# Performance work log

Measured on AMD Instinct MI355X. Metric: run time of the kernel, lower is better.

## Reference

```python
import jax, jax.numpy as jnp
import numpy as np

EPS = 1e-5  # BatchNorm2d default eps


def _deform_conv(x, offset, W_def, b_def, K):
    # torchvision.ops.DeformConv2d, stride=1, dilation=1, padding=K//2, groups=1
    B, C, H, W = x.shape
    KK = K * K
    pad = K // 2
    # offset channels ordered (y, x) per kernel tap: [B, KK, 2, H, W]
    off = offset.reshape(B, KK, 2, H, W)
    ky = (jnp.arange(KK) // K).astype(x.dtype)
    kx = (jnp.arange(KK) % K).astype(x.dtype)
    base_y = jnp.arange(H, dtype=x.dtype)[None, :, None] - pad + ky[:, None, None]  # [KK,H,1]
    base_x = jnp.arange(W, dtype=x.dtype)[None, None, :] - pad + kx[:, None, None]  # [KK,1,W]
    py = off[:, :, 0] + base_y[None]  # [B,KK,H,W] sampling rows
    px = off[:, :, 1] + base_x[None]  # [B,KK,H,W] sampling cols
    y0 = jnp.floor(py)
    x0 = jnp.floor(px)
    wy = py - y0
    wx = px - x0
    xf = x.reshape(B, C, H * W)

    def corner(iy, ix, w):
        valid = ((iy >= 0) & (iy < H) & (ix >= 0) & (ix < W)).astype(x.dtype)
        idx = jnp.clip(iy, 0, H - 1).astype(jnp.int32) * W + jnp.clip(ix, 0, W - 1).astype(jnp.int32)
        g = jnp.take_along_axis(xf, idx.reshape(B, 1, KK * H * W), axis=2)
        return g.reshape(B, C, KK, H, W) * (w * valid)[:, None]

    sampled = (corner(y0, x0, (1 - wy) * (1 - wx))
               + corner(y0, x0 + 1, (1 - wy) * wx)
               + corner(y0 + 1, x0, wy * (1 - wx))
               + corner(y0 + 1, x0 + 1, wy * wx))  # [B,C,KK,H,W]
    out = jnp.einsum('bckhw,ock->bohw', sampled, W_def.reshape(W_def.shape[0], C, KK))
    return out + b_def[None, :, None, None]


def reference(x, W_off, b_off, W_def, b_def, W_cat, b_cat, gamma, beta):
    K = W_def.shape[-1]
    # 3x3 offset-generating conv, padding=1
    offset = jax.lax.conv_general_dilated(
        x, W_off, (1, 1), ((1, 1), (1, 1)),
        dimension_numbers=('NCHW', 'OIHW', 'NCHW')) + b_off[None, :, None, None]
    y1 = _deform_conv(x, offset, W_def, b_def, K)
    # 1x1 conv
    y = jnp.einsum('bchw,oc->bohw', y1, W_cat) + b_cat[None, :, None, None]
    # BatchNorm2d in training mode (batch statistics, biased var)
    mean = y.mean(axis=(0, 2, 3))
    var = y.var(axis=(0, 2, 3))
    yn = (y - mean[None, :, None, None]) * jax.lax.rsqrt(var + EPS)[None, :, None, None]
    out = jax.nn.relu(gamma[None, :, None, None] * yn + beta[None, :, None, None])
    return out + x


def setup_inputs() -> dict:
    key = jax.random.key(0)
    ks = jax.random.split(key, 5)
    B, C, H, W, K = 4, 64, 192, 192, 3
    return {
        'x': jax.random.normal(ks[0], (B, C, H, W), dtype=jnp.float32),
        'W_off': jax.random.normal(ks[1], (2 * K * K, C, 3, 3), dtype=jnp.float32) * 0.02,
        'b_off': jnp.zeros((2 * K * K,), dtype=jnp.float32),
        'W_def': jax.random.normal(ks[2], (C, C, K, K), dtype=jnp.float32) * (1.0 / np.sqrt(C * K * K)),
        'b_def': jnp.zeros((C,), dtype=jnp.float32),
        'W_cat': jax.random.normal(ks[3], (C, C), dtype=jnp.float32) * (1.0 / np.sqrt(C)),
        'b_cat': jnp.zeros((C,), dtype=jnp.float32),
        'gamma': jnp.ones((C,), dtype=jnp.float32),
        'beta': jnp.zeros((C,), dtype=jnp.float32),
    }
```

## Files before the change

### kernel.cpp

```cpp
#include <hip/hip_runtime.h>
#include <math.h>

constexpr int Hh  = 192;
constexpr int Ww  = 192;
constexpr int HWp = Hh * Ww;
constexpr int Cc  = 64;
constexpr int Bb  = 4;
constexpr int KK  = 9;
constexpr int OFFC = 18;
constexpr int PXB = 32;
constexpr int NBPX = HWp / PXB;
constexpr int KSD = (Cc * KK) / 32;
constexpr int KSC = Cc / 32;
constexpr int NIT = KK * PXB;
constexpr int SLOTS = 64;

constexpr int NXP = Bb * (HWp / 64);
constexpr int NWP = (4 * KSD * 64 * 8 + 4 * KSC * 64 * 8 + 2 * KSD * 64 * 8) / 256;
constexpr int NZP = (2 * Cc * SLOTS / 4) / 256;

using bf16x8 = __attribute__((ext_vector_type(8))) short;
using f32x4  = __attribute__((ext_vector_type(4))) float;

static __device__ __forceinline__ unsigned short f2bf(float f) {
    unsigned int u = __float_as_uint(f);
    u += 0x7fff + ((u >> 16) & 1);
    return (unsigned short)(u >> 16);
}
static __device__ __forceinline__ float bf2f(unsigned short u) {
    return __uint_as_float((unsigned)u << 16);
}

__global__ __launch_bounds__(256)
void k_prep(const float* __restrict__ x, const float* __restrict__ Wdef,
            const float* __restrict__ Wcat, const float* __restrict__ Woff,
            unsigned short* __restrict__ xcl, unsigned short* __restrict__ Fd,
            unsigned short* __restrict__ Fc, unsigned short* __restrict__ Fo,
            float* __restrict__ psum) {
    __shared__ unsigned short tile[64][66];
    const int bid = blockIdx.x;
    const int t = threadIdx.x;
    if (bid < NXP) {
        int b   = bid / (HWp / 64);
        int px0 = (bid % (HWp / 64)) * 64;
        #pragma unroll
        for (int r = 0; r < 4; ++r) {
            int c = r * 16 + (t >> 4), px4 = (t & 15) * 4;
            float4 v = *(const float4*)(x + ((size_t)b * Cc + c) * HWp + px0 + px4);
            tile[c][px4 + 0] = f2bf(v.x);
            tile[c][px4 + 1] = f2bf(v.y);
            tile[c][px4 + 2] = f2bf(v.z);
            tile[c][px4 + 3] = f2bf(v.w);
        }
        __syncthreads();
        #pragma unroll
        for (int r = 0; r < 4; ++r) {
            int pxl = r * 16 + (t >> 4), c4 = (t & 15) * 4;
            ushort4 u;
            u.x = tile[c4 + 0][pxl];
            u.y = tile[c4 + 1][pxl];
            u.z = tile[c4 + 2][pxl];
            u.w = tile[c4 + 3][pxl];
            *(ushort4*)(xcl + ((size_t)b * HWp + px0 + pxl) * Cc + c4) = u;
        }
    } else if (bid < NXP + NWP) {
        int i = (bid - NXP) * 256 + t;
        if (i < 4 * KSD * 64 * 8) {
            int r = i & 7, lane = (i >> 3) & 63, ks = (i >> 9) % KSD, ot = (i >> 9) / KSD;
            int o  = ot * 16 + (lane & 15);
            int kp = ks * 32 + ((lane >> 4) << 3) + r;
            int kk = kp >> 6, c = kp & 63;
            Fd[i] = f2bf(Wdef[o * (Cc * KK) + c * KK + kk]);
        }
        int j = i - 4 * KSD * 64 * 8;
        if (j >= 0 && j < 4 * KSC * 64 * 8) {
            int r = j & 7, lane = (j >> 3) & 63, ks = (j >> 9) & 1, ot = j >> 10;
            int o = ot * 16 + (lane & 15);
            int c = ks * 32 + ((lane >> 4) << 3) + r;
            Fc[j] = f2bf(Wcat[o * Cc + c]);
        }
        int m = j - 4 * KSC * 64 * 8;
        if (m >= 0 && m < 2 * KSD * 64 * 8) {
            int r = m & 7, lane = (m >> 3) & 63, ks = (m >> 9) % KSD, ot = (m >> 9) / KSD;
            int o  = ot * 16 + (lane & 15);
            int kp = ks * 32 + ((lane >> 4) << 3) + r;
            int kk = kp >> 6, c = kp & 63;
            Fo[m] = (o < OFFC) ? f2bf(Woff[o * (Cc * KK) + c * KK + kk]) : 0;
        }
    } else {
        int j = (bid - NXP - NWP) * 256 + t;
        float4 z = {0.f, 0.f, 0.f, 0.f};
        ((float4*)psum)[j] = z;
    }
}

__global__ __launch_bounds__(512)
void k_fused(const unsigned short* __restrict__ xcl,
             const unsigned short* __restrict__ Fo, const float* __restrict__ boff,
             const unsigned short* __restrict__ Fd, const float* __restrict__ bdef,
             const unsigned short* __restrict__ Fc, const float* __restrict__ bcat,
             unsigned short* __restrict__ y, float* __restrict__ psum) {
    __shared__ __align__(16) unsigned char s_buf[PXB * Cc * KK * 2];
    __shared__ __align__(16) unsigned char s_y1[PXB * Cc * 2];
    __shared__ float s_off[PXB][OFFC];
    __shared__ __align__(16) int s_pp[NIT * 8];

    const int t = threadIdx.x;
    const int lane = t & 63, wv = t >> 6;
    const int klane = (lane >> 4) & 3;
    const int c4 = (lane & 15) * 4;
    int wg = blockIdx.x;
    const int slot = wg & (SLOTS - 1);
    wg = (wg & 7) * (Bb * NBPX / 8) + (wg >> 3);
    const int b   = wg / NBPX;
    const int px0 = (wg % NBPX) * PXB;
    const int h   = px0 / Ww;
    const int w0  = px0 % Ww;
    const unsigned short* xb = xcl + (size_t)b * HWp * Cc;

    #pragma unroll
    for (int it = 0; it < NIT / 32; ++it) {
        int item = it * 32 + wv * 4 + klane;
        int kk = item >> 5, pxl = item & 31;
        int ky = (kk * 11) >> 5, kx = kk - ky * 3;
        int row = h + ky - 1;
        int col = w0 + pxl + kx - 1;
        ushort4 u = {0, 0, 0, 0};
        if (row >= 0 && row < Hh && col >= 0 && col < Ww)
            u = *(const ushort4*)(xb + (size_t)(row * Ww + col) * Cc + c4);
        unsigned addr = (unsigned)pxl * (Cc * KK * 2)
                      + ((((unsigned)(kk * 64 + c4)) * 2) ^ ((unsigned)(pxl & 7) << 4));
        *(ushort4*)(s_buf + addr) = u;
    }
    __syncthreads();

    if (wv < 4) {
        const int oto = wv >> 1, pxt = wv & 1;
        const unsigned swz = (unsigned)(lane & 7) << 4;
        const unsigned rA = ((unsigned)(lane & 15) + (unsigned)pxt * 16) * (Cc * KK * 2);
        f32x4 a = {0.f, 0.f, 0.f, 0.f};
        const bf16x8* Bo = (const bf16x8*)Fo + (size_t)oto * KSD * 64;
        #pragma unroll 3
        for (int ks = 0; ks < KSD; ++ks) {
            unsigned cb = ((unsigned)(ks * 64 + klane * 16)) ^ swz;
            bf16x8 af = *(const bf16x8*)(s_buf + rA + cb);
            a = __builtin_amdgcn_mfma_f32_16x16x32_bf16(af, Bo[ks * 64 + lane], a, 0, 0, 0);
        }
        int oc = oto * 16 + (lane & 15);
        if (oc < OFFC) {
            float bv = boff[oc];
            #pragma unroll
            for (int r = 0; r < 4; ++r)
                s_off[pxt * 16 + klane * 4 + r][oc] = a[r] + bv;
        }
    }
    __syncthreads();

    if (t < NIT) {
        int i = t;
        int kk = i >> 5, pxl = i & 31;
        int ky = (kk * 11) >> 5, kx = kk - ky * 3;
        float py  = s_off[pxl][kk * 2]     + (float)(h - 1 + ky);
        float pxf = s_off[pxl][kk * 2 + 1] + (float)(w0 + pxl - 1 + kx);
        float fy0 = floorf(py), fx0 = floorf(pxf);
        float wy = py - fy0, wx = pxf - fx0;
        int iy0 = (int)fy0, ix0 = (int)fx0, iy1 = iy0 + 1, ix1 = ix0 + 1;
        float v00 = (iy0 >= 0 && iy0 < Hh && ix0 >= 0 && ix0 < Ww) ? 1.f : 0.f;
        float v01 = (iy0 >= 0 && iy0 < Hh && ix1 >= 0 && ix1 < Ww) ? 1.f : 0.f;
        float v10 = (iy1 >= 0 && iy1 < Hh && ix0 >= 0 && ix0 < Ww) ? 1.f : 0.f;
        float v11 = (iy1 >= 0 && iy1 < Hh && ix1 >= 0 && ix1 < Ww) ? 1.f : 0.f;
        int cy0 = min(max(iy0, 0), Hh - 1), cy1 = min(max(iy1, 0), Hh - 1);
        int cx0 = min(max(ix0, 0), Ww - 1), cx1 = min(max(ix1, 0), Ww - 1);
        int* pp = &s_pp[i * 8];
        pp[0] = (cy0 * Ww + cx0) * (Cc * 2);
        pp[1] = (cy0 * Ww + cx1) * (Cc * 2);
        pp[2] = (cy1 * Ww + cx0) * (Cc * 2);
        pp[3] = (cy1 * Ww + cx1) * (Cc * 2);
        pp[4] = __float_as_int((1.f - wy) * (1.f - wx) * v00);
        pp[5] = __float_as_int((1.f - wy) * wx * v01);
        pp[6] = __float_as_int(wy * (1.f - wx) * v10);
        pp[7] = __float_as_int(wy * wx * v11);
    }
    __syncthreads();

    const unsigned char* xbB = (const unsigned char*)xb + (size_t)c4 * 2;
    #pragma unroll 3
    for (int it = 0; it < NIT / 32; ++it) {
        int item = it * 32 + wv * 4 + klane;
        int kk = item >> 5, pxl = item & 31;
        const int* pp = &s_pp[item * 8];
        int4   idx = *(const int4*)pp;
        float4 wt  = *(const float4*)(pp + 4);
        ushort4 u00 = *(const ushort4*)(xbB + idx.x);
        ushort4 u01 = *(const ushort4*)(xbB + idx.y);
        ushort4 u10 = *(const ushort4*)(xbB + idx.z);
        ushort4 u11 = *(const ushort4*)(xbB + idx.w);
        float v0 = wt.x * bf2f(u00.x) + wt.y * bf2f(u01.x) + wt.z * bf2f(u10.x) + wt.w * bf2f(u11.x);
        float v1 = wt.x * bf2f(u00.y) + wt.y * bf2f(u01.y) + wt.z * bf2f(u10.y) + wt.w * bf2f(u11.y);
        float v2 = wt.x * bf2f(u00.z) + wt.y * bf2f(u01.z) + wt.z * bf2f(u10.z) + wt.w * bf2f(u11.z);
        float v3 = wt.x * bf2f(u00.w) + wt.y * bf2f(u01.w) + wt.z * bf2f(u10.w) + wt.w * bf2f(u11.w);
        ushort4 o4;
        o4.x = f2bf(v0); o4.y = f2bf(v1); o4.z = f2bf(v2); o4.w = f2bf(v3);
        unsigned addr = (unsigned)pxl * (Cc * KK * 2)
                      + ((((unsigned)(kk * 64 + c4)) * 2) ^ ((unsigned)(pxl & 7) << 4));
        *(ushort4*)(s_buf + addr) = o4;
    }
    __syncthreads();

    const int ot = wv >> 1, pxt = wv & 1;
    const unsigned swzA = (unsigned)(lane & 7) << 4;
    const unsigned rA = ((unsigned)(lane & 15) + (unsigned)pxt * 16) * (Cc * KK * 2);
    f32x4 acc = {0.f, 0.f, 0.f, 0.f};
    const bf16x8* Bd = (const bf16x8*)Fd + (size_t)ot * KSD * 64;
    #pragma unroll 3
    for (int ks = 0; ks < KSD; ++ks) {
        unsigned cb = ((unsigned)(ks * 64 + klane * 16)) ^ swzA;
        bf16x8 a0 = *(const bf16x8*)(s_buf + rA + cb);
        bf16x8 bd = Bd[ks * 64 + lane];
        acc = __builtin_amdgcn_mfma_f32_16x16x32_bf16(a0, bd, acc, 0, 0, 0);
    }
    const int o = ot * 16 + (lane & 15);
    {
        float bv = bdef[o];
        unsigned colb = (unsigned)o * 2;
        #pragma unroll
        for (int r = 0; r < 4; ++r) {
            int row = pxt * 16 + klane * 4 + r;
            unsigned sw = (unsigned)((klane * 4 + r) & 7) << 4;
            *(unsigned short*)(s_y1 + row * (Cc * 2) + (colb ^ sw)) = f2bf(acc[r] + bv);
        }
    }
    __syncthreads();

    f32x4 cacc = {0.f, 0.f, 0.f, 0.f};
    const bf16x8* Bc = (const bf16x8*)Fc + (size_t)ot * KSC * 64;
    const unsigned rY = ((unsigned)(lane & 15) + (unsigned)pxt * 16) * (Cc * 2);
    #pragma unroll
    for (int ks = 0; ks < KSC; ++ks) {
        unsigned cb = ((unsigned)(ks * 64 + klane * 16)) ^ swzA;
        bf16x8 a0 = *(const bf16x8*)(s_y1 + rY + cb);
        bf16x8 bc = Bc[ks * 64 + lane];
        cacc = __builtin_amdgcn_mfma_f32_16x16x32_bf16(a0, bc, cacc, 0, 0, 0);
    }

    float vals[4];
    {
        float bcv = bcat[o];
        #pragma unroll
        for (int r = 0; r < 4; ++r) vals[r] = cacc[r] + bcv;
        float s1 = 0.f, s2 = 0.f;
        #pragma unroll
        for (int j = 0; j < 4; ++j) { s1 += vals[j]; s2 += vals[j] * vals[j]; }
        s1 += __shfl_xor(s1, 16); s1 += __shfl_xor(s1, 32);
        s2 += __shfl_xor(s2, 16); s2 += __shfl_xor(s2, 32);
        if (klane == 0) {
            atomicAdd(&psum[o * SLOTS + slot], s1);
            atomicAdd(&psum[Cc * SLOTS + o * SLOTS + slot], s2);
        }
    }

    __syncthreads();
    {
        unsigned orow = (unsigned)o * (PXB * 4);
        unsigned sw   = (unsigned)(o & 7) << 4;
        #pragma unroll
        for (int r = 0; r < 4; ++r) {
            int p = pxt * 16 + klane * 4 + r;
            *(float*)(s_buf + orow + (((unsigned)p * 4) ^ sw)) = vals[r];
        }
    }
    __syncthreads();
    unsigned short* yb = y + (size_t)b * Cc * HWp + px0;
    {
        int oo = t >> 3, pxq = t & 7;
        float4 v = *(const float4*)(s_buf + (unsigned)oo * (PXB * 4)
                                    + (((unsigned)pxq * 16) ^ ((unsigned)(oo & 7) << 4)));
        ushort4 u;
        u.x = f2bf(v.x); u.y = f2bf(v.y); u.z = f2bf(v.z); u.w = f2bf(v.w);
        *(ushort4*)(yb + (size_t)oo * HWp + pxq * 4) = u;
    }
}

__global__ __launch_bounds__(64)
void k_stats_final(const float* __restrict__ psum, float* __restrict__ stats) {
    int c = threadIdx.x;
    double t1 = 0.0, t2 = 0.0;
    for (int s = 0; s < SLOTS; ++s) {
        t1 += (double)psum[c * SLOTS + s];
        t2 += (double)psum[Cc * SLOTS + c * SLOTS + s];
    }
    double n = (double)(Bb * HWp);
    double mean = t1 / n;
    double var  = t2 / n - mean * mean;
    stats[c]      = (float)mean;
    stats[Cc + c] = (float)(1.0 / sqrt(var + 1e-5));
}

__global__ __launch_bounds__(256)
void k_apply(const unsigned short* __restrict__ y, const float4* __restrict__ x,
             const float* __restrict__ stats, const float* __restrict__ gamma,
             const float* __restrict__ beta, float4* __restrict__ out) {
    int idx = blockIdx.x * 256 + threadIdx.x;
    int c = (idx / (HWp / 4)) % Cc;
    float mean = stats[c], inv = stats[Cc + c];
    float g = gamma[c], bt = beta[c];
    ushort4 yv = *(const ushort4*)(y + (size_t)idx * 4);
    float4 xv = x[idx], o;
    o.x = fmaxf(g * ((bf2f(yv.x) - mean) * inv) + bt, 0.f) + xv.x;
    o.y = fmaxf(g * ((bf2f(yv.y) - mean) * inv) + bt, 0.f) + xv.y;
    o.z = fmaxf(g * ((bf2f(yv.z) - mean) * inv) + bt, 0.f) + xv.z;
    o.w = fmaxf(g * ((bf2f(yv.w) - mean) * inv) + bt, 0.f) + xv.w;
    out[idx] = o;
}

extern "C" void kernel_launch(void* const* d_in, const int* in_sizes, int n_in,
                              void* d_out, int out_size, void* d_ws, size_t ws_size,
                              hipStream_t stream) {
    const float* x     = (const float*)d_in[0];
    const float* Woff  = (const float*)d_in[1];
    const float* boff  = (const float*)d_in[2];
    const float* Wdef  = (const float*)d_in[3];
    const float* bdef  = (const float*)d_in[4];
    const float* Wcat  = (const float*)d_in[5];
    const float* bcat  = (const float*)d_in[6];
    const float* gamma = (const float*)d_in[7];
    const float* beta  = (const float*)d_in[8];
    float* out = (float*)d_out;

    float* ws    = (float*)d_ws;
    float* stats = ws;
    float* psum  = stats + 128;
    unsigned short* y16 = (unsigned short*)(psum + 2 * Cc * SLOTS);
    unsigned short* Fd  = y16 + (size_t)Bb * Cc * HWp;
    unsigned short* Fc  = Fd + 4 * KSD * 64 * 8;
    unsigned short* Fo  = Fc + 4 * KSC * 64 * 8;
    unsigned short* xcl = Fo + 2 * KSD * 64 * 8;

    k_prep<<<dim3(NXP + NWP + NZP), dim3(256), 0, stream>>>(x, Wdef, Wcat, Woff,
                                                            xcl, Fd, Fc, Fo, psum);
    k_fused<<<dim3(Bb * NBPX), dim3(512), 0, stream>>>(xcl, Fo, boff, Fd, bdef, Fc, bcat, y16, psum);
    k_stats_final<<<dim3(1), dim3(64), 0, stream>>>(psum, stats);
    k_apply<<<dim3(Bb * Cc * HWp / 4 / 256), dim3(256), 0, stream>>>(
        y16, (const float4*)x, stats, gamma, beta, (float4*)out);
}
```

Baseline: 221.9 us.

## Shrink fused block to 256 threads, load halo tile, fold stats into apply

The offset conv now stages a 3x34 halo tile of x in shared memory instead of nine im2col copies, cutting global loads for that stage. The fused kernel drops from 512 to 256 threads, so each wave computes two pixel tiles for the deform and 1x1 GEMMs and reuses the B fragments. The separate stats-final kernel is removed and each apply block reduces the 64 partial sums itself. The prep transpose uses packed 32-bit swizzled shared tiles, and bilinear sampling uses 2-wide float vectors. The cost is more redundant stats reduction in apply and fewer threads to hide gather latency.

```diff
diff --git a/kernel.cpp b/kernel.cpp
--- a/kernel.cpp
+++ b/kernel.cpp
@@ -14,6 +14,8 @@
 constexpr int KSC = Cc / 32;
 constexpr int NIT = KK * PXB;
 constexpr int SLOTS = 64;
+constexpr int XT_COLS = PXB + 2;
+constexpr int XT_ITEMS = 3 * XT_COLS;
 
 constexpr int NXP = Bb * (HWp / 64);
 constexpr int NWP = (4 * KSD * 64 * 8 + 4 * KSC * 64 * 8 + 2 * KSD * 64 * 8) / 256;
@@ -21,6 +23,7 @@
 
 using bf16x8 = __attribute__((ext_vector_type(8))) short;
 using f32x4  = __attribute__((ext_vector_type(4))) float;
+using f32x2  = __attribute__((ext_vector_type(2))) float;
 
 static __device__ __forceinline__ unsigned short f2bf(float f) {
     unsigned int u = __float_as_uint(f);
@@ -37,7 +40,7 @@
             unsigned short* __restrict__ xcl, unsigned short* __restrict__ Fd,
             unsigned short* __restrict__ Fc, unsigned short* __restrict__ Fo,
             float* __restrict__ psum) {
-    __shared__ unsigned short tile[64][66];
+    __shared__ unsigned int wtile[64][32];
     const int bid = blockIdx.x;
     const int t = threadIdx.x;
     if (bid < NXP) {
@@ -45,23 +48,29 @@
         int px0 = (bid % (HWp / 64)) * 64;
         #pragma unroll
         for (int r = 0; r < 4; ++r) {
-            int c = r * 16 + (t >> 4), px4 = (t & 15) * 4;
-            float4 v = *(const float4*)(x + ((size_t)b * Cc + c) * HWp + px0 + px4);
-            tile[c][px4 + 0] = f2bf(v.x);
-            tile[c][px4 + 1] = f2bf(v.y);
-            tile[c][px4 + 2] = f2bf(v.z);
-            tile[c][px4 + 3] = f2bf(v.w);
+            int cc = r * 16 + (t >> 4), px4 = (t & 15) * 4;
+            float4 v = *(const float4*)(x + ((size_t)b * Cc + cc) * HWp + px0 + px4);
+            unsigned lo  = (unsigned)f2bf(v.x) | ((unsigned)f2bf(v.y) << 16);
+            unsigned hi2 = (unsigned)f2bf(v.z) | ((unsigned)f2bf(v.w) << 16);
+            unsigned e = (unsigned)(cc & 31);
+            wtile[cc][((unsigned)(px4 >> 1)    ) ^ e] = lo;
+            wtile[cc][((unsigned)(px4 >> 1) + 1) ^ e] = hi2;
         }
         __syncthreads();
         #pragma unroll
         for (int r = 0; r < 4; ++r) {
-            int pxl = r * 16 + (t >> 4), c4 = (t & 15) * 4;
+            int pxl = r * 16 + (t >> 4), c4l = (t & 15) * 4;
+            int hsel = (pxl & 1) * 16;
+            unsigned w0 = wtile[c4l + 0][(unsigned)(pxl >> 1) ^ (unsigned)((c4l + 0) & 31)];
+            unsigned w1 = wtile[c4l + 1][(unsigned)(pxl >> 1) ^ (unsigned)((c4l + 1) & 31)];
+            unsigned w2 = wtile[c4l + 2][(unsigned)(pxl >> 1) ^ (unsigned)((c4l + 2) & 31)];
+            unsigned w3 = wtile[c4l + 3][(unsigned)(pxl >> 1) ^ (unsigned)((c4l + 3) & 31)];
             ushort4 u;
-            u.x = tile[c4 + 0][pxl];
-            u.y = tile[c4 + 1][pxl];
-            u.z = tile[c4 + 2][pxl];
-            u.w = tile[c4 + 3][pxl];
-            *(ushort4*)(xcl + ((size_t)b * HWp + px0 + pxl) * Cc + c4) = u;
+            u.x = (unsigned short)(w0 >> hsel);
+            u.y = (unsigned short)(w1 >> hsel);
+            u.z = (unsigned short)(w2 >> hsel);
+            u.w = (unsigned short)(w3 >> hsel);
+            *(ushort4*)(xcl + ((size_t)b * HWp + px0 + pxl) * Cc + c4l) = u;
         }
     } else if (bid < NXP + NWP) {
         int i = (bid - NXP) * 256 + t;
@@ -94,7 +103,7 @@
     }
 }
 
-__global__ __launch_bounds__(512)
+__global__ __launch_bounds__(256, 3)
 void k_fused(const unsigned short* __restrict__ xcl,
              const unsigned short* __restrict__ Fo, const float* __restrict__ boff,
              const unsigned short* __restrict__ Fd, const float* __restrict__ bdef,
@@ -119,31 +128,34 @@
     const unsigned short* xb = xcl + (size_t)b * HWp * Cc;
 
     #pragma unroll
-    for (int it = 0; it < NIT / 32; ++it) {
-        int item = it * 32 + wv * 4 + klane;
-        int kk = item >> 5, pxl = item & 31;
-        int ky = (kk * 11) >> 5, kx = kk - ky * 3;
-        int row = h + ky - 1;
-        int col = w0 + pxl + kx - 1;
-        ushort4 u = {0, 0, 0, 0};
-        if (row >= 0 && row < Hh && col >= 0 && col < Ww)
-            u = *(const ushort4*)(xb + (size_t)(row * Ww + col) * Cc + c4);
-        unsigned addr = (unsigned)pxl * (Cc * KK * 2)
-                      + ((((unsigned)(kk * 64 + c4)) * 2) ^ ((unsigned)(pxl & 7) << 4));
-        *(ushort4*)(s_buf + addr) = u;
-    }
-    __syncthreads();
-
-    if (wv < 4) {
-        const int oto = wv >> 1, pxt = wv & 1;
-        const unsigned swz = (unsigned)(lane & 7) << 4;
-        const unsigned rA = ((unsigned)(lane & 15) + (unsigned)pxt * 16) * (Cc * KK * 2);
+    for (int it = 0; it < 7; ++it) {
+        int item = it * 16 + wv * 4 + klane;
+        if (item < XT_ITEMS) {
+            int ry = item / XT_COLS, cx = item - ry * XT_COLS;
+            int row = h + ry - 1, col = w0 + cx - 1;
+            ushort4 u = {0, 0, 0, 0};
+            if (row >= 0 && row < Hh && col >= 0 && col < Ww)
+                u = *(const ushort4*)(xb + (size_t)(row * Ww + col) * Cc + c4);
+            unsigned addr = (unsigned)item * 128
+                          + (((unsigned)c4 * 2) ^ (((unsigned)item & 7) << 4));
+            *(ushort4*)(s_buf + addr) = u;
+        }
+    }
+    __syncthreads();
+
+    {
+        const int oto = wv >> 1, pxt0 = wv & 1;
+        const int pxv = (lane & 15) + pxt0 * 16;
         f32x4 a = {0.f, 0.f, 0.f, 0.f};
         const bf16x8* Bo = (const bf16x8*)Fo + (size_t)oto * KSD * 64;
-        #pragma unroll 3
+        #pragma unroll
         for (int ks = 0; ks < KSD; ++ks) {
-            unsigned cb = ((unsigned)(ks * 64 + klane * 16)) ^ swz;
-            bf16x8 af = *(const bf16x8*)(s_buf + rA + cb);
+            const int kk = ks >> 1;
+            const int ky = kk / 3, kx = kk % 3;
+            int row_l = ky * XT_COLS + pxv + kx;
+            unsigned c0b = (unsigned)(((ks & 1) * 32 + klane * 8) * 2);
+            unsigned addr = (unsigned)row_l * 128 + (c0b ^ (((unsigned)row_l & 7) << 4));
+            bf16x8 af = *(const bf16x8*)(s_buf + addr);
             a = __builtin_amdgcn_mfma_f32_16x16x32_bf16(af, Bo[ks * 64 + lane], a, 0, 0, 0);
         }
         int oc = oto * 16 + (lane & 15);
@@ -151,13 +163,12 @@
             float bv = boff[oc];
             #pragma unroll
             for (int r = 0; r < 4; ++r)
-                s_off[pxt * 16 + klane * 4 + r][oc] = a[r] + bv;
-        }
-    }
-    __syncthreads();
-
-    if (t < NIT) {
-        int i = t;
+                s_off[pxt0 * 16 + klane * 4 + r][oc] = a[r] + bv;
+        }
+    }
+    __syncthreads();
+
+    for (int i = t; i < NIT; i += 256) {
         int kk = i >> 5, pxl = i & 31;
         int ky = (kk * 11) >> 5, kx = kk - ky * 3;
         float py  = s_off[pxl][kk * 2]     + (float)(h - 1 + ky);
@@ -184,9 +195,9 @@
     __syncthreads();
 
     const unsigned char* xbB = (const unsigned char*)xb + (size_t)c4 * 2;
-    #pragma unroll 3
-    for (int it = 0; it < NIT / 32; ++it) {
-        int item = it * 32 + wv * 4 + klane;
+    #pragma unroll 6
+    for (int it = 0; it < NIT / 16; ++it) {
+        int item = it * 16 + wv * 4 + klane;
         int kk = item >> 5, pxl = item & 31;
         const int* pp = &s_pp[item * 8];
         int4   idx = *(const int4*)pp;
@@ -195,29 +206,34 @@
         ushort4 u01 = *(const ushort4*)(xbB + idx.y);
         ushort4 u10 = *(const ushort4*)(xbB + idx.z);
         ushort4 u11 = *(const ushort4*)(xbB + idx.w);
-        float v0 = wt.x * bf2f(u00.x) + wt.y * bf2f(u01.x) + wt.z * bf2f(u10.x) + wt.w * bf2f(u11.x);
-        float v1 = wt.x * bf2f(u00.y) + wt.y * bf2f(u01.y) + wt.z * bf2f(u10.y) + wt.w * bf2f(u11.y);
-        float v2 = wt.x * bf2f(u00.z) + wt.y * bf2f(u01.z) + wt.z * bf2f(u10.z) + wt.w * bf2f(u11.z);
-        float v3 = wt.x * bf2f(u00.w) + wt.y * bf2f(u01.w) + wt.z * bf2f(u10.w) + wt.w * bf2f(u11.w);
+        f32x2 lo00 = {bf2f(u00.x), bf2f(u00.y)}, hi00 = {bf2f(u00.z), bf2f(u00.w)};
+        f32x2 lo01 = {bf2f(u01.x), bf2f(u01.y)}, hi01 = {bf2f(u01.z), bf2f(u01.w)};
+        f32x2 lo10 = {bf2f(u10.x), bf2f(u10.y)}, hi10 = {bf2f(u10.z), bf2f(u10.w)};
+        f32x2 lo11 = {bf2f(u11.x), bf2f(u11.y)}, hi11 = {bf2f(u11.z), bf2f(u11.w)};
+        f32x2 vlo = wt.x * lo00 + wt.y * lo01 + wt.z * lo10 + wt.w * lo11;
+        f32x2 vhi = wt.x * hi00 + wt.y * hi01 + wt.z * hi10 + wt.w * hi11;
         ushort4 o4;
-        o4.x = f2bf(v0); o4.y = f2bf(v1); o4.z = f2bf(v2); o4.w = f2bf(v3);
+        o4.x = f2bf(vlo[0]); o4.y = f2bf(vlo[1]); o4.z = f2bf(vhi[0]); o4.w = f2bf(vhi[1]);
         unsigned addr = (unsigned)pxl * (Cc * KK * 2)
                       + ((((unsigned)(kk * 64 + c4)) * 2) ^ ((unsigned)(pxl & 7) << 4));
         *(ushort4*)(s_buf + addr) = o4;
     }
     __syncthreads();
 
-    const int ot = wv >> 1, pxt = wv & 1;
+    const int ot = wv;
     const unsigned swzA = (unsigned)(lane & 7) << 4;
-    const unsigned rA = ((unsigned)(lane & 15) + (unsigned)pxt * 16) * (Cc * KK * 2);
-    f32x4 acc = {0.f, 0.f, 0.f, 0.f};
+    const unsigned rA0  = (unsigned)(lane & 15) * (Cc * KK * 2);
+    const unsigned rA1  = rA0 + 16u * (Cc * KK * 2);
+    f32x4 acc0 = {0.f, 0.f, 0.f, 0.f}, acc1 = {0.f, 0.f, 0.f, 0.f};
     const bf16x8* Bd = (const bf16x8*)Fd + (size_t)ot * KSD * 64;
     #pragma unroll 3
     for (int ks = 0; ks < KSD; ++ks) {
         unsigned cb = ((unsigned)(ks * 64 + klane * 16)) ^ swzA;
-        bf16x8 a0 = *(const bf16x8*)(s_buf + rA + cb);
+        bf16x8 a0 = *(const bf16x8*)(s_buf + rA0 + cb);
+        bf16x8 a1 = *(const bf16x8*)(s_buf + rA1 + cb);
         bf16x8 bd = Bd[ks * 64 + lane];
-        acc = __builtin_amdgcn_mfma_f32_16x16x32_bf16(a0, bd, acc, 0, 0, 0);
+        acc0 = __builtin_amdgcn_mfma_f32_16x16x32_bf16(a0, bd, acc0, 0, 0, 0);
+        acc1 = __builtin_amdgcn_mfma_f32_16x16x32_bf16(a1, bd, acc1, 0, 0, 0);
     }
     const int o = ot * 16 + (lane & 15);
     {
@@ -225,32 +241,36 @@
         unsigned colb = (unsigned)o * 2;
         #pragma unroll
         for (int r = 0; r < 4; ++r) {
-            int row = pxt * 16 + klane * 4 + r;
-            unsigned sw = (unsigned)((klane * 4 + r) & 7) << 4;
-            *(unsigned short*)(s_y1 + row * (Cc * 2) + (colb ^ sw)) = f2bf(acc[r] + bv);
-        }
-    }
-    __syncthreads();
-
-    f32x4 cacc = {0.f, 0.f, 0.f, 0.f};
+            int row0 = klane * 4 + r, row1 = row0 + 16;
+            unsigned sw = (unsigned)(row0 & 7) << 4;
+            *(unsigned short*)(s_y1 + row0 * (Cc * 2) + (colb ^ sw)) = f2bf(acc0[r] + bv);
+            *(unsigned short*)(s_y1 + row1 * (Cc * 2) + (colb ^ sw)) = f2bf(acc1[r] + bv);
+        }
+    }
+    __syncthreads();
+
+    f32x4 c0 = {0.f, 0.f, 0.f, 0.f}, c1 = {0.f, 0.f, 0.f, 0.f};
     const bf16x8* Bc = (const bf16x8*)Fc + (size_t)ot * KSC * 64;
-    const unsigned rY = ((unsigned)(lane & 15) + (unsigned)pxt * 16) * (Cc * 2);
+    const unsigned rY0 = (unsigned)(lane & 15) * (Cc * 2);
+    const unsigned rY1 = rY0 + 16u * (Cc * 2);
     #pragma unroll
     for (int ks = 0; ks < KSC; ++ks) {
         unsigned cb = ((unsigned)(ks * 64 + klane * 16)) ^ swzA;
-        bf16x8 a0 = *(const bf16x8*)(s_y1 + rY + cb);
+        bf16x8 a0 = *(const bf16x8*)(s_y1 + rY0 + cb);
+        bf16x8 a1 = *(const bf16x8*)(s_y1 + rY1 + cb);
         bf16x8 bc = Bc[ks * 64 + lane];
-        cacc = __builtin_amdgcn_mfma_f32_16x16x32_bf16(a0, bc, cacc, 0, 0, 0);
-    }
-
-    float vals[4];
+        c0 = __builtin_amdgcn_mfma_f32_16x16x32_bf16(a0, bc, c0, 0, 0, 0);
+        c1 = __builtin_amdgcn_mfma_f32_16x16x32_bf16(a1, bc, c1, 0, 0, 0);
+    }
+
+    float vals[8];
     {
         float bcv = bcat[o];
         #pragma unroll
-        for (int r = 0; r < 4; ++r) vals[r] = cacc[r] + bcv;
+        for (int r = 0; r < 4; ++r) { vals[r] = c0[r] + bcv; vals[4 + r] = c1[r] + bcv; }
         float s1 = 0.f, s2 = 0.f;
         #pragma unroll
-        for (int j = 0; j < 4; ++j) { s1 += vals[j]; s2 += vals[j] * vals[j]; }
+        for (int j = 0; j < 8; ++j) { s1 += vals[j]; s2 += vals[j] * vals[j]; }
         s1 += __shfl_xor(s1, 16); s1 += __shfl_xor(s1, 32);
         s2 += __shfl_xor(s2, 16); s2 += __shfl_xor(s2, 32);
         if (klane == 0) {
@@ -265,14 +285,16 @@
         unsigned sw   = (unsigned)(o & 7) << 4;
         #pragma unroll
         for (int r = 0; r < 4; ++r) {
-            int p = pxt * 16 + klane * 4 + r;
-            *(float*)(s_buf + orow + (((unsigned)p * 4) ^ sw)) = vals[r];
+            int p0 = klane * 4 + r, p1 = p0 + 16;
+            *(float*)(s_buf + orow + (((unsigned)p0 * 4) ^ sw)) = vals[r];
+            *(float*)(s_buf + orow + (((unsigned)p1 * 4) ^ sw)) = vals[4 + r];
         }
     }
     __syncthreads();
     unsigned short* yb = y + (size_t)b * Cc * HWp + px0;
-    {
-        int oo = t >> 3, pxq = t & 7;
+    #pragma unroll
+    for (int it = 0; it < 2; ++it) {
+        int oo = it * 32 + (t >> 3), pxq = t & 7;
         float4 v = *(const float4*)(s_buf + (unsigned)oo * (PXB * 4)
                                     + (((unsigned)pxq * 16) ^ ((unsigned)(oo & 7) << 4)));
         ushort4 u;
@@ -281,28 +303,32 @@
     }
 }
 
-__global__ __launch_bounds__(64)
-void k_stats_final(const float* __restrict__ psum, float* __restrict__ stats) {
-    int c = threadIdx.x;
-    double t1 = 0.0, t2 = 0.0;
-    for (int s = 0; s < SLOTS; ++s) {
-        t1 += (double)psum[c * SLOTS + s];
-        t2 += (double)psum[Cc * SLOTS + c * SLOTS + s];
-    }
-    double n = (double)(Bb * HWp);
-    double mean = t1 / n;
-    double var  = t2 / n - mean * mean;
-    stats[c]      = (float)mean;
-    stats[Cc + c] = (float)(1.0 / sqrt(var + 1e-5));
-}
-
 __global__ __launch_bounds__(256)
 void k_apply(const unsigned short* __restrict__ y, const float4* __restrict__ x,
-             const float* __restrict__ stats, const float* __restrict__ gamma,
+             const float* __restrict__ psum, const float* __restrict__ gamma,
              const float* __restrict__ beta, float4* __restrict__ out) {
-    int idx = blockIdx.x * 256 + threadIdx.x;
-    int c = (idx / (HWp / 4)) % Cc;
-    float mean = stats[c], inv = stats[Cc + c];
+    __shared__ float smv[2];
+    const int t = threadIdx.x;
+    const int idx = blockIdx.x * 256 + t;
+    const int c = (blockIdx.x * 1024 / HWp) % Cc;
+    if (t < 64) {
+        float s1 = psum[c * SLOTS + t];
+        float s2 = psum[Cc * SLOTS + c * SLOTS + t];
+        #pragma unroll
+        for (int d = 1; d < 64; d <<= 1) {
+            s1 += __shfl_xor(s1, d);
+            s2 += __shfl_xor(s2, d);
+        }
+        if (t == 0) {
+            float n = (float)(Bb * HWp);
+            float mean = s1 / n;
+            float var  = s2 / n - mean * mean;
+            smv[0] = mean;
+            smv[1] = 1.0f / sqrtf(var + 1e-5f);
+        }
+    }
+    __syncthreads();
+    float mean = smv[0], inv = smv[1];
     float g = gamma[c], bt = beta[c];
     ushort4 yv = *(const ushort4*)(y + (size_t)idx * 4);
     float4 xv = x[idx], o;
@@ -328,8 +354,7 @@
     float* out = (float*)d_out;
 
     float* ws    = (float*)d_ws;
-    float* stats = ws;
-    float* psum  = stats + 128;
+    float* psum  = ws;
     unsigned short* y16 = (unsigned short*)(psum + 2 * Cc * SLOTS);
     unsigned short* Fd  = y16 + (size_t)Bb * Cc * HWp;
     unsigned short* Fc  = Fd + 4 * KSD * 64 * 8;
@@ -338,8 +363,7 @@
 
     k_prep<<<dim3(NXP + NWP + NZP), dim3(256), 0, stream>>>(x, Wdef, Wcat, Woff,
                                                             xcl, Fd, Fc, Fo, psum);
-    k_fused<<<dim3(Bb * NBPX), dim3(512), 0, stream>>>(xcl, Fo, boff, Fd, bdef, Fc, bcat, y16, psum);
-    k_stats_final<<<dim3(1), dim3(64), 0, stream>>>(psum, stats);
+    k_fused<<<dim3(Bb * NBPX), dim3(256), 0, stream>>>(xcl, Fo, boff, Fd, bdef, Fc, bcat, y16, psum);
     k_apply<<<dim3(Bb * Cc * HWp / 4 / 256), dim3(256), 0, stream>>>(
-        y16, (const float4*)x, stats, gamma, beta, (float4*)out);
-}
+        y16, (const float4*)x, psum, gamma, beta, (float4*)out);
+}
```

Measured after the change: 207.2 us. 6.6% less time.
